# Kernel tuning notes

Hardware: AMD Instinct MI355X
Metric: run time of the kernel (lower is better)

Reference implementation:

```python
import jax, jax.numpy as jnp
import numpy as np

B, T, I, H, C = 8192, 28, 28, 128, 10


def setup_inputs() -> dict:
    key = jax.random.key(0)
    ks = jax.random.split(key, 7)
    s_ih = 1.0 / np.sqrt(H)
    return {
        "x": jax.random.normal(ks[0], (B, T, I), dtype=jnp.float32),
        "W_ih": jax.random.normal(ks[1], (4 * H, I), dtype=jnp.float32) * s_ih,
        "W_hh": jax.random.normal(ks[2], (4 * H, H), dtype=jnp.float32) * s_ih,
        "b_ih": jax.random.normal(ks[3], (4 * H,), dtype=jnp.float32) * s_ih,
        "b_hh": jax.random.normal(ks[4], (4 * H,), dtype=jnp.float32) * s_ih,
        "W_fc": jax.random.normal(ks[5], (C, H), dtype=jnp.float32) * s_ih,
        "b_fc": jnp.zeros((C,), dtype=jnp.float32),
    }


def reference(x, W_ih, W_hh, b_ih, b_hh, W_fc, b_fc):
    # x: [B, T, I]. PyTorch LSTM gate order: i, f, g, o.
    b = b_ih + b_hh  # [4H]
    # Precompute input projections for all timesteps: [T, B, 4H]
    x_proj = jnp.einsum("bti,gi->tbg", x, W_ih) + b
    h0 = jnp.zeros((x.shape[0], H), dtype=x.dtype)
    c0 = jnp.zeros_like(h0)

    def step(carry, xp_t):
        h, c = carry
        gates = xp_t + h @ W_hh.T  # [B, 4H]
        i_g, f_g, g_g, o_g = jnp.split(gates, 4, axis=-1)
        i_g = jax.nn.sigmoid(i_g)
        f_g = jax.nn.sigmoid(f_g)
        g_g = jnp.tanh(g_g)
        o_g = jax.nn.sigmoid(o_g)
        c = f_g * c + i_g * g_g
        h = o_g * jnp.tanh(c)
        return (h, c), None

    (h_last, _), _ = jax.lax.scan(step, (h0, c0), x_proj)
    # outputs[:, -1, :] == final hidden state; fc + relu
    return jax.nn.relu(h_last @ W_fc.T + b_fc)
```

## Files before the change

### kernel.cpp

```cpp
#include <hip/hip_runtime.h>
#include <math.h>

typedef __attribute__((ext_vector_type(8))) _Float16 half8;
typedef __attribute__((ext_vector_type(4))) _Float16 half4;
typedef __attribute__((ext_vector_type(4))) float    f32x4;

#define TSTEPS 28
#define IDIM   28
#define HDIM   128
#define NKC    5
#define TILE_B 16
#define CDIM   10

#if __has_builtin(__builtin_amdgcn_exp2f)
#define EXP2F(x) __builtin_amdgcn_exp2f(x)
#else
#define EXP2F(x) exp2f(x)
#endif
#if __has_builtin(__builtin_amdgcn_rcpf)
#define RCPF(x) __builtin_amdgcn_rcpf(x)
#else
#define RCPF(x) (1.0f / (x))
#endif

__global__ __launch_bounds__(256) void pack_w(const float* __restrict__ Wih,
                                              const float* __restrict__ Whh,
                                              _Float16* __restrict__ P) {
    int e = blockIdx.x * 256 + threadIdx.x;
    if (e >= NKC * 4 * 8 * 64 * 8) return;
    int j  = e & 7;
    int ln = (e >> 3) & 63;
    int w  = (e >> 9) & 7;
    int t  = (e >> 12) & 3;
    int kc = e >> 14;
    int k  = kc * 32 + ((ln >> 4) << 3) + j;
    int u  = w * 16 + (ln & 15);
    int g  = t * HDIM + u;
    float v = 0.f;
    if (k < HDIM)              v = Whh[g * HDIM + k];
    else if (k < HDIM + IDIM)  v = Wih[g * IDIM + (k - HDIM)];
    P[e] = (_Float16)v;
}

__global__ __launch_bounds__(512, 4) void lstm_kernel(
    const float* __restrict__ x,
    const _Float16* __restrict__ P,
    const float* __restrict__ b_ih, const float* __restrict__ b_hh,
    const float* __restrict__ Wfc,
    const float* __restrict__ b_fc,
    float* __restrict__ out)
{
    __shared__ __align__(16) _Float16 frag[NKC][64][8];
    __shared__ __align__(16) _Float16 Plds[4][8][64][8];
    __shared__ __align__(16) float hplain[TILE_B][HDIM + 4];

    const int tid = threadIdx.x;
    const int l   = tid & 63;
    const int w   = tid >> 6;
    const int b0  = blockIdx.x * TILE_B;
    const int u   = w * 16 + (l & 15);

    {
        const float4* P4 = (const float4*)P;
        float4* dst = (float4*)Plds;
        #pragma unroll
        for (int q = 0; q < 4; ++q)
            dst[tid + q * 512] = P4[8192 + tid + q * 512];
    }
    half8 breg[4][4];
    {
        const half8* Pp = (const half8*)P;
        #pragma unroll
        for (int kc = 0; kc < 4; ++kc)
            #pragma unroll
            for (int t4 = 0; t4 < 4; ++t4)
                breg[t4][kc] = Pp[((kc * 4 + t4) * 8 + w) * 64 + l];
    }
    float biasv[4];
    #pragma unroll
    for (int t4 = 0; t4 < 4; ++t4)
        biasv[t4] = b_ih[t4 * HDIM + u] + b_hh[t4 * HDIM + u];

    {
        float4 z = {0.f, 0.f, 0.f, 0.f};
        ((float4*)frag)[tid] = z;
        if (tid < 16) {
            half4 zh = {(_Float16)0.f, (_Float16)0.f, (_Float16)0.f, (_Float16)0.f};
            *(half4*)&frag[4][48 + tid][4] = zh;
        }
    }
    const int xrow = tid / 7, xg = tid % 7;
    if (tid < 112) {
        float4 xv = ((const float4*)(x + ((size_t)(b0 + xrow) * TSTEPS + 0) * IDIM))[xg];
        half4 hv = {(_Float16)xv.x, (_Float16)xv.y, (_Float16)xv.z, (_Float16)xv.w};
        *(half4*)&frag[4][xrow + 16 * (xg >> 1)][(xg & 1) * 4] = hv;
    }

    float cst[4] = {0.f, 0.f, 0.f, 0.f};
    const int kc_h = w >> 1;
    const int quad = (2 * w + ((l >> 3) & 1)) & 3;
    const int jh   = l & 7;

    __syncthreads();

    for (int t = 0; t < TSTEPS; ++t) {
        float4 xv;
        const bool doload = (t + 1 < TSTEPS) && (tid < 112);
        if (doload)
            xv = ((const float4*)(x + ((size_t)(b0 + xrow) * TSTEPS + (t + 1)) * IDIM))[xg];

        f32x4 acc[4];
        #pragma unroll
        for (int t4 = 0; t4 < 4; ++t4) {
            f32x4 a4 = {biasv[t4], biasv[t4], biasv[t4], biasv[t4]};
            acc[t4] = a4;
        }

        #pragma unroll
        for (int kc = 0; kc < NKC; ++kc) {
            half8 a = *(const half8*)&frag[kc][l][0];
            if (kc < 4) {
                acc[0] = __builtin_amdgcn_mfma_f32_16x16x32_f16(a, breg[0][kc], acc[0], 0, 0, 0);
                acc[1] = __builtin_amdgcn_mfma_f32_16x16x32_f16(a, breg[1][kc], acc[1], 0, 0, 0);
                acc[2] = __builtin_amdgcn_mfma_f32_16x16x32_f16(a, breg[2][kc], acc[2], 0, 0, 0);
                acc[3] = __builtin_amdgcn_mfma_f32_16x16x32_f16(a, breg[3][kc], acc[3], 0, 0, 0);
            } else {
                #pragma unroll
                for (int t4 = 0; t4 < 4; ++t4) {
                    half8 b = *(const half8*)&Plds[t4][w][l][0];
                    acc[t4] = __builtin_amdgcn_mfma_f32_16x16x32_f16(a, b, acc[t4], 0, 0, 0);
                }
            }
        }
        __syncthreads();

        #pragma unroll
        for (int r = 0; r < 4; ++r) {
            int m = ((l >> 4) << 2) + r;
            float ig = acc[0][r], fg = acc[1][r], gg = acc[2][r], og = acc[3][r];
            float is = RCPF(1.f + EXP2F(ig * -1.44269504f));
            float fs = RCPF(1.f + EXP2F(fg * -1.44269504f));
            float os = RCPF(1.f + EXP2F(og * -1.44269504f));
            float gt = 1.f - 2.f * RCPF(1.f + EXP2F(gg * 2.88539008f));
            float c  = fs * cst[r] + is * gt;
            cst[r] = c;
            float tc = 1.f - 2.f * RCPF(1.f + EXP2F(c * 2.88539008f));
            float h  = os * tc;
            frag[kc_h][m + 16 * quad][jh] = (_Float16)h;
            if (t == TSTEPS - 1) hplain[m][u] = h;
        }
        if (doload) {
            half4 hv = {(_Float16)xv.x, (_Float16)xv.y, (_Float16)xv.z, (_Float16)xv.w};
            *(half4*)&frag[4][xrow + 16 * (xg >> 1)][(xg & 1) * 4] = hv;
        }
        __syncthreads();
    }

    if (tid < TILE_B * CDIM) {
        int row = tid / CDIM, c = tid % CDIM;
        const float4* hv = (const float4*)&hplain[row][0];
        const float4* wf = (const float4*)(Wfc + c * HDIM);
        float s = b_fc[c];
        #pragma unroll
        for (int q = 0; q < 32; ++q) {
            float4 a = hv[q], b = wf[q];
            s += a.x * b.x + a.y * b.y + a.z * b.z + a.w * b.w;
        }
        out[(size_t)(b0 + row) * CDIM + c] = fmaxf(s, 0.f);
    }
}

extern "C" void kernel_launch(void* const* d_in, const int* in_sizes, int n_in,
                              void* d_out, int out_size, void* d_ws, size_t ws_size,
                              hipStream_t stream) {
    const float* x   = (const float*)d_in[0];
    const float* Wih = (const float*)d_in[1];
    const float* Whh = (const float*)d_in[2];
    const float* bih = (const float*)d_in[3];
    const float* bhh = (const float*)d_in[4];
    const float* Wfc = (const float*)d_in[5];
    const float* bfc = (const float*)d_in[6];
    float* out = (float*)d_out;
    _Float16* P = (_Float16*)d_ws;

    hipLaunchKernelGGL(pack_w, dim3(320), dim3(256), 0, stream, Wih, Whh, P);
    hipLaunchKernelGGL(lstm_kernel, dim3(8192 / TILE_B), dim3(512), 0, stream,
                       x, P, bih, bhh, Wfc, bfc, out);
}
```

Baseline: 132.4 us.

## Double-buffer LSTM state fragments and fold activation scales into weights

Double-buffers the shared h/x fragment buffer so each timestep reads one buffer and writes the other. This removes one of the two block barriers per step. It also pre-multiplies the packed weights and biases by -log2(e), or 2*log2(e) for the g gate, so the gate nonlinearities skip a multiply per element. The cost is a second fragment buffer in LDS, which may reduce occupancy, and fp16 rounding now applies to the scaled weights.

Result: faster. 127.5 us (-3.7%).

```diff
diff --git a/kernel.cpp b/kernel.cpp
--- a/kernel.cpp
+++ b/kernel.cpp
@@ -23,6 +23,9 @@
 #define RCPF(x) (1.0f / (x))
 #endif
 
+#define NLOG2E (-1.44269504f)
+#define P2LOG2E (2.88539008f)
+
 __global__ __launch_bounds__(256) void pack_w(const float* __restrict__ Wih,
                                               const float* __restrict__ Whh,
                                               _Float16* __restrict__ P) {
@@ -39,7 +42,8 @@
     float v = 0.f;
     if (k < HDIM)              v = Whh[g * HDIM + k];
     else if (k < HDIM + IDIM)  v = Wih[g * IDIM + (k - HDIM)];
-    P[e] = (_Float16)v;
+    float sc = (t == 2) ? P2LOG2E : NLOG2E;
+    P[e] = (_Float16)(v * sc);
 }
 
 __global__ __launch_bounds__(512, 4) void lstm_kernel(
@@ -50,7 +54,7 @@
     const float* __restrict__ b_fc,
     float* __restrict__ out)
 {
-    __shared__ __align__(16) _Float16 frag[NKC][64][8];
+    __shared__ __align__(16) _Float16 frag[2][NKC][64][8];
     __shared__ __align__(16) _Float16 Plds[4][8][64][8];
     __shared__ __align__(16) float hplain[TILE_B][HDIM + 4];
 
@@ -78,22 +82,25 @@
     }
     float biasv[4];
     #pragma unroll
-    for (int t4 = 0; t4 < 4; ++t4)
-        biasv[t4] = b_ih[t4 * HDIM + u] + b_hh[t4 * HDIM + u];
+    for (int t4 = 0; t4 < 4; ++t4) {
+        float sc = (t4 == 2) ? P2LOG2E : NLOG2E;
+        biasv[t4] = (b_ih[t4 * HDIM + u] + b_hh[t4 * HDIM + u]) * sc;
+    }
 
     {
         float4 z = {0.f, 0.f, 0.f, 0.f};
-        ((float4*)frag)[tid] = z;
-        if (tid < 16) {
+        if (tid < 256) ((float4*)&frag[0][0][0][0])[tid] = z;
+        if (tid < 32) {
+            int b = tid >> 4, i = tid & 15;
             half4 zh = {(_Float16)0.f, (_Float16)0.f, (_Float16)0.f, (_Float16)0.f};
-            *(half4*)&frag[4][48 + tid][4] = zh;
+            *(half4*)&frag[b][4][48 + i][4] = zh;
         }
     }
     const int xrow = tid / 7, xg = tid % 7;
     if (tid < 112) {
         float4 xv = ((const float4*)(x + ((size_t)(b0 + xrow) * TSTEPS + 0) * IDIM))[xg];
         half4 hv = {(_Float16)xv.x, (_Float16)xv.y, (_Float16)xv.z, (_Float16)xv.w};
-        *(half4*)&frag[4][xrow + 16 * (xg >> 1)][(xg & 1) * 4] = hv;
+        *(half4*)&frag[0][4][xrow + 16 * (xg >> 1)][(xg & 1) * 4] = hv;
     }
 
     float cst[4] = {0.f, 0.f, 0.f, 0.f};
@@ -103,7 +110,7 @@
 
     __syncthreads();
 
-    for (int t = 0; t < TSTEPS; ++t) {
+    auto step = [&](int t, _Float16 (*cur)[64][8], _Float16 (*nxt)[64][8]) {
         float4 xv;
         const bool doload = (t + 1 < TSTEPS) && (tid < 112);
         if (doload)
@@ -118,7 +125,7 @@
 
         #pragma unroll
         for (int kc = 0; kc < NKC; ++kc) {
-            half8 a = *(const half8*)&frag[kc][l][0];
+            half8 a = *(const half8*)&cur[kc][l][0];
             if (kc < 4) {
                 acc[0] = __builtin_amdgcn_mfma_f32_16x16x32_f16(a, breg[0][kc], acc[0], 0, 0, 0);
                 acc[1] = __builtin_amdgcn_mfma_f32_16x16x32_f16(a, breg[1][kc], acc[1], 0, 0, 0);
@@ -132,28 +139,31 @@
                 }
             }
         }
-        __syncthreads();
 
         #pragma unroll
         for (int r = 0; r < 4; ++r) {
             int m = ((l >> 4) << 2) + r;
-            float ig = acc[0][r], fg = acc[1][r], gg = acc[2][r], og = acc[3][r];
-            float is = RCPF(1.f + EXP2F(ig * -1.44269504f));
-            float fs = RCPF(1.f + EXP2F(fg * -1.44269504f));
-            float os = RCPF(1.f + EXP2F(og * -1.44269504f));
-            float gt = 1.f - 2.f * RCPF(1.f + EXP2F(gg * 2.88539008f));
+            float is = RCPF(1.f + EXP2F(acc[0][r]));
+            float fs = RCPF(1.f + EXP2F(acc[1][r]));
+            float os = RCPF(1.f + EXP2F(acc[3][r]));
+            float gt = 1.f - 2.f * RCPF(1.f + EXP2F(acc[2][r]));
             float c  = fs * cst[r] + is * gt;
             cst[r] = c;
-            float tc = 1.f - 2.f * RCPF(1.f + EXP2F(c * 2.88539008f));
+            float tc = 1.f - 2.f * RCPF(1.f + EXP2F(c * P2LOG2E));
             float h  = os * tc;
-            frag[kc_h][m + 16 * quad][jh] = (_Float16)h;
+            nxt[kc_h][m + 16 * quad][jh] = (_Float16)h;
             if (t == TSTEPS - 1) hplain[m][u] = h;
         }
         if (doload) {
             half4 hv = {(_Float16)xv.x, (_Float16)xv.y, (_Float16)xv.z, (_Float16)xv.w};
-            *(half4*)&frag[4][xrow + 16 * (xg >> 1)][(xg & 1) * 4] = hv;
+            *(half4*)&nxt[4][xrow + 16 * (xg >> 1)][(xg & 1) * 4] = hv;
         }
         __syncthreads();
+    };
+
+    for (int tt = 0; tt < TSTEPS; tt += 2) {
+        step(tt,     frag[0], frag[1]);
+        step(tt + 1, frag[1], frag[0]);
     }
 
     if (tid < TILE_B * CDIM) {
```
